# Kernel tuning notes

Measured on AMD Instinct MI355X. Metric: run time of the kernel, lower is better.

## Reference

```python
import jax, jax.numpy as jnp
import numpy as np

B, H, W = 32, 256, 512
C, HF, WF = 768, 16, 32
MAX_KP = 512
NMS_RADIUS = 3.0
SCORE_THRESH = 0.1
K_CAND = min(MAX_KP * 4, H * W)  # 2048


def setup_inputs() -> dict:
    key = jax.random.key(0)
    k1, k2 = jax.random.split(key)
    gray_image = jax.random.uniform(k1, (B, 1, H, W), dtype=jnp.float32)
    mask = jnp.ones((B, 1, H, W), dtype=jnp.float32)
    feat_map = jax.random.normal(k2, (B, C, HF, WF), dtype=jnp.float32)
    return {"gray_image": gray_image, "mask": mask, "feat_map": feat_map}


def _detect_and_sample(img, m, fm):
    # img, m: (H, W); fm: (C, HF, WF)
    masked = (img * m).reshape(-1)
    vals, idx = jax.lax.top_k(masked, K_CAND)  # sorted descending, like torch.topk
    x = (idx % W).astype(jnp.float32)
    y = (idx // W).astype(jnp.float32)
    kp = jnp.stack([x, y], axis=1)  # (K, 2)
    valid = vals > SCORE_THRESH

    # Sequential greedy NMS over score-sorted candidates (matches the torch loop)
    ar = jnp.arange(K_CAND)

    def body(i, keep):
        di = jnp.sqrt(jnp.sum((kp - kp[i]) ** 2, axis=1))
        suppress = (ar > i) & (di < NMS_RADIUS)
        return jnp.where(keep[i], keep & ~suppress, keep)

    keep = jax.lax.fori_loop(0, K_CAND, body, valid)

    # Compact kept points to the front (stable, preserves score order), pad to MAX_KP
    order = jnp.argsort(jnp.logical_not(keep), stable=True)
    sel = order[:MAX_KP]
    n_keep = jnp.sum(keep)
    ok = (jnp.arange(MAX_KP) < n_keep).astype(vals.dtype)  # 1 for real kps, 0 for pad
    kp_out = kp[sel] * ok[:, None]
    sc_out = vals[sel] * ok

    # grid_sample: bilinear, align_corners=True, padding_mode='border'
    # grid = 2*x/W_img - 1  ->  fx = (grid+1)/2*(WF-1) = x/W_img*(WF-1)
    fx = kp_out[:, 0] / W * (WF - 1)
    fy = kp_out[:, 1] / H * (HF - 1)
    x0f, y0f = jnp.floor(fx), jnp.floor(fy)
    wx, wy = fx - x0f, fy - y0f
    x0 = jnp.clip(x0f, 0, WF - 1).astype(jnp.int32)
    x1 = jnp.clip(x0f + 1, 0, WF - 1).astype(jnp.int32)
    y0 = jnp.clip(y0f, 0, HF - 1).astype(jnp.int32)
    y1 = jnp.clip(y0f + 1, 0, HF - 1).astype(jnp.int32)
    g = lambda yy, xx: fm[:, yy, xx]  # (C, MAX_KP)
    desc = (g(y0, x0) * (1 - wx) * (1 - wy) + g(y0, x1) * wx * (1 - wy)
            + g(y1, x0) * (1 - wx) * wy + g(y1, x1) * wx * wy)
    return kp_out, sc_out, desc.T  # (MAX_KP,2), (MAX_KP,), (MAX_KP,C)


def reference(gray_image, mask, feat_map):
    kp, sc, desc = jax.vmap(_detect_and_sample)(gray_image[:, 0], mask[:, 0], feat_map)
    return kp, sc, desc
```

## Files before the change

### kernel.cpp

```cpp
#include <hip/hip_runtime.h>

#define HW_TOT 131072
#define IMG_W  512
#define IMG_H  256
#define KC     2048
#define MAXKP  512
#define NB     32
#define NC     768
#define CG     32
#define NCG    (NC / CG)
#define NBUCK  2048
#define NFB    4096
#define NCAND  4096
#define NSEG   8
#define SEGSZ  (HW_TOT / NSEG)
#define SEGCAP 1024
#define VT0    0.975f
#define LSTRIDE 514
#define MPRE   1024

typedef float f32x4 __attribute__((ext_vector_type(4)));

#define SEGCNT_OFF 0
#define CAND_OFF   2048

__device__ __forceinline__ int blockExclScan(int s, int tid, int* wsum)
{
    const int lane = tid & 63, wid = tid >> 6;
    int incl = s;
    #pragma unroll
    for (int d = 1; d < 64; d <<= 1) {
        int t = __shfl_up(incl, d);
        if (lane >= d) incl += t;
    }
    if (lane == 63) wsum[wid] = incl;
    __syncthreads();
    if (tid == 0) {
        int run = 0;
        #pragma unroll
        for (int w = 0; w < 16; ++w) { int c = wsum[w]; wsum[w] = run; run += c; }
    }
    __syncthreads();
    return wsum[wid] + incl - s;
}

__global__ __launch_bounds__(1024) void scan1_kernel(
    const float* __restrict__ gray,
    const float* __restrict__ mask,
    unsigned int* __restrict__ segcnt,
    unsigned long long* __restrict__ cand)
{
    const int b   = blockIdx.x >> 3;
    const int seg = blockIdx.x & 7;
    const int tid = threadIdx.x;

    __shared__ unsigned long long st[SEGCAP];
    __shared__ unsigned int lcnt;
    if (tid == 0) lcnt = 0u;
    __syncthreads();

    const float4* gi = (const float4*)(gray + (size_t)b * HW_TOT + (size_t)seg * SEGSZ);
    const float4* mi = (const float4*)(mask + (size_t)b * HW_TOT + (size_t)seg * SEGSZ);
    for (int e = tid; e < SEGSZ / 4; e += 1024) {
        float4 g = gi[e], m = mi[e];
        float vv[4] = { g.x * m.x, g.y * m.y, g.z * m.z, g.w * m.w };
        #pragma unroll
        for (int c = 0; c < 4; ++c) {
            float v = vv[c];
            if (v >= VT0) {
                unsigned int eg = (unsigned int)(seg * SEGSZ + 4 * e + c);
                unsigned int p  = atomicAdd(&lcnt, 1u);
                if (p < SEGCAP)
                    st[p] = ((unsigned long long)__float_as_uint(v) << 32) |
                            (unsigned long long)(~eg);
            }
        }
    }
    __syncthreads();
    if (tid == 0) segcnt[blockIdx.x] = lcnt;
    const unsigned int n = lcnt < SEGCAP ? lcnt : SEGCAP;
    unsigned long long* cb = cand + (size_t)blockIdx.x * SEGCAP;
    for (unsigned int i = tid; i < n; i += 1024) cb[i] = st[i];
}

__global__ __launch_bounds__(1024) void final_kernel(
    const float* __restrict__ gray,
    const float* __restrict__ mask,
    const unsigned long long* __restrict__ cand,
    const unsigned int* __restrict__ segcnt,
    float* __restrict__ out_kp,
    float* __restrict__ out_sc)
{
    const int b   = blockIdx.x;
    const int tid = threadIdx.x;

    __shared__ unsigned long long sorted[NCAND];
    __shared__ unsigned long long BUF0[NFB / 2];
    __shared__ unsigned long long BUF1[NFB / 2];
    __shared__ unsigned int posArr[KC];
    __shared__ float valArr[KC];
    __shared__ unsigned int segoff[NSEG + 1];
    __shared__ int wsum[16];
    __shared__ int shT;
    __shared__ unsigned int flagSh;

    unsigned int* cntB   = (unsigned int*)BUF0;
    unsigned int* startB = (unsigned int*)BUF1;

    if (tid == 0) {
        unsigned int tot = 0; int bad = 0; unsigned int run = 0;
        #pragma unroll
        for (int sg = 0; sg < NSEG; ++sg) {
            unsigned int c = segcnt[b * NSEG + sg];
            if (c > SEGCAP) bad = 1;
            segoff[sg] = run; run += c; tot += c;
        }
        segoff[NSEG] = run;
        if (tot < KC || tot > NCAND) bad = 1;
        flagSh = (unsigned int)bad;
        shT = 0;
    }
    __syncthreads();
    const int flag = (int)flagSh;

    const float4* gi = (const float4*)(gray + (size_t)b * HW_TOT);
    const float4* mi = (const float4*)(mask + (size_t)b * HW_TOT);

    if (flag) {
        unsigned int* lh = (unsigned int*)BUF0;
        for (int i = tid; i < NBUCK; i += 1024) lh[i] = 0u;
        __syncthreads();
        for (int e = tid; e < HW_TOT / 4; e += 1024) {
            float4 g = gi[e], m = mi[e];
            int b0 = (int)(g.x * m.x * 2048.0f); b0 = b0 > 2047 ? 2047 : b0;
            int b1 = (int)(g.y * m.y * 2048.0f); b1 = b1 > 2047 ? 2047 : b1;
            int b2 = (int)(g.z * m.z * 2048.0f); b2 = b2 > 2047 ? 2047 : b2;
            int b3 = (int)(g.w * m.w * 2048.0f); b3 = b3 > 2047 ? 2047 : b3;
            atomicAdd(&lh[b0], 1u); atomicAdd(&lh[b1], 1u);
            atomicAdd(&lh[b2], 1u); atomicAdd(&lh[b3], 1u);
        }
        __syncthreads();
        int c0v = (int)lh[2047 - 2 * tid];
        int c1v = (int)lh[2046 - 2 * tid];
        int ex  = blockExclScan(c0v + c1v, tid, wsum);
        int cmax = -1;
        if (ex + c0v >= KC)            cmax = 2047 - 2 * tid;
        else if (ex + c0v + c1v >= KC) cmax = 2046 - 2 * tid;
        if (cmax >= 0) atomicMax(&shT, cmax);
        __syncthreads();
    }
    const float lo    = flag ? (float)shT * (1.0f / 2048.0f) : VT0;
    const float scale = (float)NFB / (1.0f - lo);

    for (int i = tid; i < NFB; i += 1024) cntB[i] = 0u;
    sorted[tid] = 0ull; sorted[tid + 1024] = 0ull;
    __syncthreads();

    if (!flag) {
        for (int sg = 0; sg < NSEG; ++sg) {
            const int n = (int)(segoff[sg + 1] - segoff[sg]);
            const unsigned long long* cbs = cand + (size_t)(b * NSEG + sg) * SEGCAP;
            for (int i = tid; i < n; i += 1024) {
                float v = __uint_as_float((unsigned int)(cbs[i] >> 32));
                int bk = (int)((v - lo) * scale);
                bk = bk < 0 ? 0 : (bk > NFB - 1 ? NFB - 1 : bk);
                atomicAdd(&cntB[bk], 1u);
            }
        }
    } else {
        for (int e = tid; e < HW_TOT / 4; e += 1024) {
            float4 g = gi[e], m = mi[e];
            float vv[4] = { g.x * m.x, g.y * m.y, g.z * m.z, g.w * m.w };
            #pragma unroll
            for (int c = 0; c < 4; ++c) {
                float v = vv[c];
                if (v >= lo) {
                    int bk = (int)((v - lo) * scale);
                    bk = bk < 0 ? 0 : (bk > NFB - 1 ? NFB - 1 : bk);
                    atomicAdd(&cntB[bk], 1u);
                }
            }
        }
    }
    __syncthreads();

    {
        int c[4]; int s = 0;
        #pragma unroll
        for (int j = 0; j < 4; ++j) { c[j] = (int)cntB[NFB - 1 - (4 * tid + j)]; s += c[j]; }
        int ex = blockExclScan(s, tid, wsum);
        #pragma unroll
        for (int j = 0; j < 4; ++j) { startB[NFB - 1 - (4 * tid + j)] = (unsigned int)ex; ex += c[j]; }
    }
    __syncthreads();

    if (!flag) {
        for (int sg = 0; sg < NSEG; ++sg) {
            const int n = (int)(segoff[sg + 1] - segoff[sg]);
            const unsigned long long* cbs = cand + (size_t)(b * NSEG + sg) * SEGCAP;
            for (int i = tid; i < n; i += 1024) {
                unsigned long long key = cbs[i];
                float v = __uint_as_float((unsigned int)(key >> 32));
                int bk = (int)((v - lo) * scale);
                bk = bk < 0 ? 0 : (bk > NFB - 1 ? NFB - 1 : bk);
                unsigned int p = atomicAdd(&startB[bk], 1u);
                if (p < NCAND) sorted[p] = key;
            }
        }
    } else {
        for (int e = tid; e < HW_TOT / 4; e += 1024) {
            float4 g = gi[e], m = mi[e];
            float vv[4] = { g.x * m.x, g.y * m.y, g.z * m.z, g.w * m.w };
            #pragma unroll
            for (int c = 0; c < 4; ++c) {
                float v = vv[c];
                if (v >= lo) {
                    unsigned int eg = (unsigned int)(4 * e + c);
                    int bk = (int)((v - lo) * scale);
                    bk = bk < 0 ? 0 : (bk > NFB - 1 ? NFB - 1 : bk);
                    unsigned int p = atomicAdd(&startB[bk], 1u);
                    if (p < NCAND)
                        sorted[p] = ((unsigned long long)__float_as_uint(v) << 32) |
                                    (unsigned long long)(~eg);
                }
            }
        }
    }
    __syncthreads();

    for (int k = tid; k < NFB; k += 1024) {
        int n = (int)cntB[k];
        if (n >= 2) {
            int endp = (int)startB[k];
            int s    = endp - n;
            if (s < KC) {
                int e2 = endp < NCAND ? endp : NCAND;
                for (int a = s + 1; a < e2; ++a) {
                    unsigned long long key = sorted[a];
                    int bp = a - 1;
                    while (bp >= s && sorted[bp] < key) { sorted[bp + 1] = sorted[bp]; --bp; }
                    sorted[bp + 1] = key;
                }
            }
        }
    }
    __syncthreads();

    for (int i = tid; i < KC; i += 1024) {
        unsigned long long key = sorted[i];
        posArr[i] = ~((unsigned int)(key & 0xFFFFFFFFull));
        valArr[i] = __uint_as_float((unsigned int)(key >> 32));
    }
    __syncthreads();

    unsigned int*   cellCnt   = (unsigned int*)BUF0;
    unsigned int*   cellStart = cellCnt + 2048;
    unsigned short* cellList  = (unsigned short*)BUF1;
    unsigned char*  keepA     = (unsigned char*)(cellList + 2048);
    unsigned char*  keepB     = keepA + KC;
    unsigned char*  nbrCnt    = keepB + KC;
    unsigned short* nbrList   = (unsigned short*)sorted;

    int myKeep = 0;
    int usedPrefix = 1;

    {
        const int i = tid;
        const unsigned int e = posArr[i];
        const int x = (int)(e & (IMG_W - 1)), y = (int)(e >> 9);
        const int cx = (x >> 3) & 63, cy = (y >> 3) & 31;
        const int cell = cy * 64 + cx;
        const bool valid = (valArr[i] > 0.1f);

        cellCnt[tid] = 0u; cellCnt[tid + 1024] = 0u;
        __syncthreads();
        atomicAdd(&cellCnt[cell], 1u);
        __syncthreads();
        {
            int c0v = (int)cellCnt[2 * tid], c1v = (int)cellCnt[2 * tid + 1];
            int ex = blockExclScan(c0v + c1v, tid, wsum);
            cellStart[2 * tid]     = (unsigned int)ex;
            cellStart[2 * tid + 1] = (unsigned int)(ex + c0v);
        }
        __syncthreads();
        {
            unsigned int p = atomicAdd(&cellStart[cell], 1u);
            cellList[p] = (unsigned short)i;
        }
        __syncthreads();

        int n = 0;
        bool sup1 = false;
        for (int dy = -1; dy <= 1; ++dy) {
            int cyy = cy + dy; if (cyy < 0 || cyy > 31) continue;
            for (int dx = -1; dx <= 1; ++dx) {
                int cxx = cx + dx; if (cxx < 0 || cxx > 63) continue;
                int cc = cyy * 64 + cxx;
                int end = (int)cellStart[cc], num = (int)cellCnt[cc];
                for (int q = end - num; q < end; ++q) {
                    int j = (int)cellList[q];
                    if (j < i) {
                        unsigned int ej = posArr[j];
                        int ddx = x - (int)(ej & (IMG_W - 1));
                        int ddy = y - (int)(ej >> 9);
                        if (ddx * ddx + ddy * ddy < 9) {
                            if (n < 8) nbrList[i * 8 + n] = (unsigned short)j;
                            ++n;
                            sup1 = sup1 || (valArr[j] > 0.1f);
                        }
                    }
                }
            }
        }
        nbrCnt[i] = (unsigned char)(n > 8 ? 9 : n);
        int cur = (valid && !sup1) ? 1 : 0;
        keepA[i] = (unsigned char)cur;
        __syncthreads();

        unsigned char *curK = keepA, *nxtK = keepB;
        for (int it = 0; it < KC; ++it) {
            int nv = 0;
            if (valid) {
                bool sup = false;
                int nn = (int)nbrCnt[i];
                if (nn <= 8) {
                    for (int q = 0; q < nn; ++q) sup = sup || (curK[nbrList[i * 8 + q]] != 0);
                } else {
                    for (int dy = -1; dy <= 1 && !sup; ++dy) {
                        int cyy = cy + dy; if (cyy < 0 || cyy > 31) continue;
                        for (int dx = -1; dx <= 1 && !sup; ++dx) {
                            int cxx = cx + dx; if (cxx < 0 || cxx > 63) continue;
                            int cc = cyy * 64 + cxx;
                            int end = (int)cellStart[cc], num = (int)cellCnt[cc];
                            for (int q = end - num; q < end; ++q) {
                                int j = (int)cellList[q];
                                if (j < i && curK[j]) {
                                    unsigned int ej = posArr[j];
                                    int ddx = x - (int)(ej & (IMG_W - 1));
                                    int ddy = y - (int)(ej >> 9);
                                    if (ddx * ddx + ddy * ddy < 9) { sup = true; break; }
                                }
                            }
                        }
                    }
                }
                nv = sup ? 0 : 1;
            }
            nxtK[i] = (unsigned char)nv;
            int totCh = __syncthreads_count(nv != cur);
            { unsigned char* t = curK; curK = nxtK; nxtK = t; }
            cur = nv;
            if (totCh == 0) break;
        }
        myKeep = cur;

        int keeps = __syncthreads_count(myKeep);
        if (keeps < MAXKP) usedPrefix = 0;
    }

    unsigned char* finK = keepA;
    if (!usedPrefix) {
        __syncthreads();
        for (int i = tid; i < 2048; i += 1024) cellCnt[i] = 0u;
        __syncthreads();
        for (int i = tid; i < KC; i += 1024) {
            unsigned int e = posArr[i];
            int cell = (int)((((e >> 9) >> 3) & 31u) * 64u + (((e & (IMG_W-1)) >> 3) & 63u));
            atomicAdd(&cellCnt[cell], 1u);
        }
        __syncthreads();
        {
            int c0v = (int)cellCnt[2 * tid], c1v = (int)cellCnt[2 * tid + 1];
            int ex = blockExclScan(c0v + c1v, tid, wsum);
            cellStart[2 * tid]     = (unsigned int)ex;
            cellStart[2 * tid + 1] = (unsigned int)(ex + c0v);
        }
        __syncthreads();
        for (int i = tid; i < KC; i += 1024) {
            unsigned int e = posArr[i];
            int cell = (int)((((e >> 9) >> 3) & 31u) * 64u + (((e & (IMG_W-1)) >> 3) & 63u));
            unsigned int p = atomicAdd(&cellStart[cell], 1u);
            cellList[p] = (unsigned short)i;
        }
        __syncthreads();
        for (int i = tid; i < KC; i += 1024) {
            unsigned int e = posArr[i];
            int x = (int)(e & (IMG_W - 1)), y = (int)(e >> 9);
            int cx = (x >> 3) & 63, cy = (y >> 3) & 31;
            int n = 0; bool sup1 = false;
            for (int dy = -1; dy <= 1; ++dy) {
                int cyy = cy + dy; if (cyy < 0 || cyy > 31) continue;
                for (int dx = -1; dx <= 1; ++dx) {
                    int cxx = cx + dx; if (cxx < 0 || cxx > 63) continue;
                    int cc = cyy * 64 + cxx;
                    int end = (int)cellStart[cc], num = (int)cellCnt[cc];
                    for (int q = end - num; q < end; ++q) {
                        int j = (int)cellList[q];
                        if (j < i) {
                            unsigned int ej = posArr[j];
                            int ddx = x - (int)(ej & (IMG_W - 1));
                            int ddy = y - (int)(ej >> 9);
                            if (ddx * ddx + ddy * ddy < 9) {
                                if (n < 8) nbrList[i * 8 + n] = (unsigned short)j;
                                ++n;
                                sup1 = sup1 || (valArr[j] > 0.1f);
                            }
                        }
                    }
                }
            }
            nbrCnt[i] = (unsigned char)(n > 8 ? 9 : n);
            keepA[i]  = ((valArr[i] > 0.1f) && !sup1) ? 1 : 0;
        }
        __syncthreads();
        unsigned char *curK = keepA, *nxtK = keepB;
        for (int it = 0; it < KC; ++it) {
            int localCh = 0;
            for (int i = tid; i < KC; i += 1024) {
                unsigned char c0 = curK[i];
                unsigned char nv = 0;
                if (valArr[i] > 0.1f) {
                    int nn = (int)nbrCnt[i];
                    bool sup = false;
                    if (nn <= 8) {
                        for (int q = 0; q < nn; ++q) sup = sup || (curK[nbrList[i * 8 + q]] != 0);
                    } else {
                        unsigned int e = posArr[i];
                        int x = (int)(e & (IMG_W - 1)), y = (int)(e >> 9);
                        int cx = (x >> 3) & 63, cy = (y >> 3) & 31;
                        for (int dy = -1; dy <= 1 && !sup; ++dy) {
                            int cyy = cy + dy; if (cyy < 0 || cyy > 31) continue;
                            for (int dx = -1; dx <= 1 && !sup; ++dx) {
                                int cxx = cx + dx; if (cxx < 0 || cxx > 63) continue;
                                int cc = cyy * 64 + cxx;
                                int end = (int)cellStart[cc], num = (int)cellCnt[cc];
                                for (int q = end - num; q < end; ++q) {
                                    int j = (int)cellList[q];
                                    if (j < i && curK[j]) {
                                        unsigned int ej = posArr[j];
                                        int ddx = x - (int)(ej & (IMG_W - 1));
                                        int ddy = y - (int)(ej >> 9);
                                        if (ddx * ddx + ddy * ddy < 9) { sup = true; break; }
                                    }
                                }
                            }
                        }
                    }
                    nv = sup ? 0 : 1;
                }
                nxtK[i] = nv;
                localCh |= (nv != c0);
            }
            int totCh = __syncthreads_count(localCh);
            { unsigned char* t = curK; curK = nxtK; nxtK = t; }
            if (totCh == 0) break;
        }
        finK = curK;
    }

    float* kpb = out_kp + (size_t)b * (MAXKP * 2);
    float* scb = out_sc + (size_t)b * MAXKP;

    int a0, a1, i0, i1;
    if (usedPrefix) { i0 = tid;     i1 = -1;          a0 = myKeep;         a1 = 0; }
    else            { i0 = 2 * tid; i1 = 2 * tid + 1; a0 = (int)finK[i0]; a1 = (int)finK[i1]; }
    int ex = blockExclScan(a0 + a1, tid, wsum);
    int r0 = ex, r1 = ex + a0;

    if (tid < MAXKP) { kpb[2 * tid] = 0.f; kpb[2 * tid + 1] = 0.f; scb[tid] = 0.f; }
    __syncthreads();
    if (a0 && r0 < MAXKP) {
        unsigned int e = posArr[i0];
        kpb[2 * r0] = (float)(e & (IMG_W - 1)); kpb[2 * r0 + 1] = (float)(e >> 9);
        scb[r0] = valArr[i0];
    }
    if (a1 && r1 < MAXKP) {
        unsigned int e = posArr[i1];
        kpb[2 * r1] = (float)(e & (IMG_W - 1)); kpb[2 * r1 + 1] = (float)(e >> 9);
        scb[r1] = valArr[i1];
    }
}

__global__ __launch_bounds__(1024) void sample_kernel(
    const float* __restrict__ fm,
    const float* __restrict__ kp,
    float* __restrict__ out_desc)
{
    const int blk = blockIdx.x;
    const int b   = blk / NCG;
    const int cg  = blk % NCG;
    const int c0  = cg * CG;
    const int tid = threadIdx.x;

    __shared__ float L[CG * LSTRIDE];
    __shared__ float sxl[MAXKP], syl[MAXKP];

    const float4* src = (const float4*)(fm + (size_t)b * NC * 512 + (size_t)c0 * 512);
    #pragma unroll
    for (int it = 0; it < 4; ++it) {
        int e  = tid + it * 1024;
        int cc = e >> 7, j = e & 127;
        float4 v = src[cc * 128 + j];
        float* dst = &L[cc * LSTRIDE + 4 * j];
        *(float2*)(dst)     = make_float2(v.x, v.y);
        *(float2*)(dst + 2) = make_float2(v.z, v.w);
    }
    if (tid < MAXKP) {
        float2 k2 = ((const float2*)kp)[(size_t)b * MAXKP + tid];
        sxl[tid] = k2.x; syl[tid] = k2.y;
    }
    __syncthreads();

    const int chunk = tid & 7;
    float* outb = out_desc + (size_t)b * MAXKP * NC + c0 + 4 * chunk;
    #pragma unroll
    for (int it = 0; it < 4; ++it) {
        const int p = it * 128 + (tid >> 3);
        float x = sxl[p], y = syl[p];
        float fx = x * (31.0f / 512.0f);
        float fy = y * (15.0f / 256.0f);
        float x0f = floorf(fx), y0f = floorf(fy);
        float wx = fx - x0f, wy = fy - y0f;
        int x0 = (int)fminf(x0f,       31.f);
        int x1 = (int)fminf(x0f + 1.f, 31.f);
        int y0 = (int)fminf(y0f,       15.f);
        int y1 = (int)fminf(y0f + 1.f, 15.f);
        float w00 = (1.f - wx) * (1.f - wy);
        float w01 = wx * (1.f - wy);
        float w10 = (1.f - wx) * wy;
        float w11 = wx * wy;
        int o00 = y0 * 32 + x0, o01 = y0 * 32 + x1;
        int o10 = y1 * 32 + x0, o11 = y1 * 32 + x1;

        f32x4 r;
        #pragma unroll
        for (int u = 0; u < 4; ++u) {
            const float* Lc = &L[(4 * chunk + u) * LSTRIDE];
            r[u] = Lc[o00] * w00 + Lc[o01] * w01 + Lc[o10] * w10 + Lc[o11] * w11;
        }
        __builtin_nontemporal_store(r, (f32x4*)(outb + (size_t)p * NC));
    }
}

extern "C" void kernel_launch(void* const* d_in, const int* in_sizes, int n_in,
                              void* d_out, int out_size, void* d_ws, size_t ws_size,
                              hipStream_t stream)
{
    const float* gray = (const float*)d_in[0];
    const float* mask = (const float*)d_in[1];
    const float* fm   = (const float*)d_in[2];

    float* out      = (float*)d_out;
    float* out_kp   = out;
    float* out_sc   = out + (size_t)NB * MAXKP * 2;
    float* out_desc = out + (size_t)NB * MAXKP * 2 + (size_t)NB * MAXKP;

    unsigned int*       segcnt = (unsigned int*)((char*)d_ws + SEGCNT_OFF);
    unsigned long long* cand   = (unsigned long long*)((char*)d_ws + CAND_OFF);

    scan1_kernel <<<NB * NSEG, 1024, 0, stream>>>(gray, mask, segcnt, cand);
    final_kernel <<<NB,        1024, 0, stream>>>(gray, mask, cand, segcnt,
                                                  out_kp, out_sc);
    sample_kernel<<<NB * NCG,  1024, 0, stream>>>(fm, out_kp, out_desc);
}
```

Before: 50.30 us.

## Fuse keypoint selection into descriptor sampling kernel with redundant per-block NMS

Merges the per-image selection/NMS kernel into the descriptor sampling kernel, so every channel-group block recomputes the keypoints for its image and samples directly from shared memory. This removes one kernel launch and the global round-trip for keypoints, and fills the GPU with many more blocks. In exchange, the selection work is duplicated across channel groups. Shared memory is also reduced by halving the fine bucket count and the neighbor list width, which may push more points onto slower fallback paths.

Measured after the change: 86.13 us. +71.3%, slower.

```diff
diff --git a/kernel.cpp b/kernel.cpp
--- a/kernel.cpp
+++ b/kernel.cpp
@@ -10,14 +10,14 @@
 #define CG     32
 #define NCG    (NC / CG)
 #define NBUCK  2048
-#define NFB    4096
+#define NFB    2048
 #define NCAND  4096
 #define NSEG   8
 #define SEGSZ  (HW_TOT / NSEG)
 #define SEGCAP 1024
 #define VT0    0.975f
 #define LSTRIDE 514
-#define MPRE   1024
+#define NBRW   4
 
 typedef float f32x4 __attribute__((ext_vector_type(4)));
 
@@ -83,29 +83,34 @@
     for (unsigned int i = tid; i < n; i += 1024) cb[i] = st[i];
 }
 
-__global__ __launch_bounds__(1024) void final_kernel(
+__global__ __launch_bounds__(1024) void fused_kernel(
     const float* __restrict__ gray,
     const float* __restrict__ mask,
+    const float* __restrict__ fm,
     const unsigned long long* __restrict__ cand,
     const unsigned int* __restrict__ segcnt,
     float* __restrict__ out_kp,
-    float* __restrict__ out_sc)
+    float* __restrict__ out_sc,
+    float* __restrict__ out_desc)
 {
-    const int b   = blockIdx.x;
+    const int blk = blockIdx.x;
+    const int b   = blk / NCG;
+    const int cg  = blk % NCG;
+    const int c0  = cg * CG;
     const int tid = threadIdx.x;
 
-    __shared__ unsigned long long sorted[NCAND];
-    __shared__ unsigned long long BUF0[NFB / 2];
-    __shared__ unsigned long long BUF1[NFB / 2];
-    __shared__ unsigned int posArr[KC];
-    __shared__ float valArr[KC];
+    __shared__ char U[CG * LSTRIDE * 4];
+    __shared__ float sxl[MAXKP], syl[MAXKP], sss[MAXKP];
     __shared__ unsigned int segoff[NSEG + 1];
     __shared__ int wsum[16];
     __shared__ int shT;
     __shared__ unsigned int flagSh;
 
-    unsigned int* cntB   = (unsigned int*)BUF0;
-    unsigned int* startB = (unsigned int*)BUF1;
+    unsigned long long* sorted = (unsigned long long*)U;
+    unsigned int* cntB   = (unsigned int*)(U + 32768);
+    unsigned int* startB = (unsigned int*)(U + 40960);
+    unsigned int* posArr = (unsigned int*)(U + 49152);
+    float*        valArr = (float*)(U + 57344);
 
     if (tid == 0) {
         unsigned int tot = 0; int bad = 0; unsigned int run = 0;
@@ -127,7 +132,7 @@
     const float4* mi = (const float4*)(mask + (size_t)b * HW_TOT);
 
     if (flag) {
-        unsigned int* lh = (unsigned int*)BUF0;
+        unsigned int* lh = cntB;
         for (int i = tid; i < NBUCK; i += 1024) lh[i] = 0u;
         __syncthreads();
         for (int e = tid; e < HW_TOT / 4; e += 1024) {
@@ -185,12 +190,11 @@
     __syncthreads();
 
     {
-        int c[4]; int s = 0;
-        #pragma unroll
-        for (int j = 0; j < 4; ++j) { c[j] = (int)cntB[NFB - 1 - (4 * tid + j)]; s += c[j]; }
-        int ex = blockExclScan(s, tid, wsum);
-        #pragma unroll
-        for (int j = 0; j < 4; ++j) { startB[NFB - 1 - (4 * tid + j)] = (unsigned int)ex; ex += c[j]; }
+        int c0v = (int)cntB[NFB - 1 - 2 * tid];
+        int c1v = (int)cntB[NFB - 2 - 2 * tid];
+        int ex  = blockExclScan(c0v + c1v, tid, wsum);
+        startB[NFB - 1 - 2 * tid] = (unsigned int)ex;
+        startB[NFB - 2 - 2 * tid] = (unsigned int)(ex + c0v);
     }
     __syncthreads();
 
@@ -253,17 +257,16 @@
     }
     __syncthreads();
 
-    unsigned int*   cellCnt   = (unsigned int*)BUF0;
-    unsigned int*   cellStart = cellCnt + 2048;
-    unsigned short* cellList  = (unsigned short*)BUF1;
-    unsigned char*  keepA     = (unsigned char*)(cellList + 2048);
-    unsigned char*  keepB     = keepA + KC;
-    unsigned char*  nbrCnt    = keepB + KC;
-    unsigned short* nbrList   = (unsigned short*)sorted;
+    unsigned int*   cellCnt   = cntB;
+    unsigned int*   cellStart = startB;
+    unsigned short* nbrList   = (unsigned short*)U;
+    unsigned short* cellList  = (unsigned short*)(U + 16384);
+    unsigned char*  keepA     = (unsigned char*)(U + 20480);
+    unsigned char*  keepB     = (unsigned char*)(U + 22528);
+    unsigned char*  nbrCnt    = (unsigned char*)(U + 24576);
 
     int myKeep = 0;
     int usedPrefix = 1;
-
     {
         const int i = tid;
         const unsigned int e = posArr[i];
@@ -304,7 +307,7 @@
                         int ddx = x - (int)(ej & (IMG_W - 1));
                         int ddy = y - (int)(ej >> 9);
                         if (ddx * ddx + ddy * ddy < 9) {
-                            if (n < 8) nbrList[i * 8 + n] = (unsigned short)j;
+                            if (n < NBRW) nbrList[i * NBRW + n] = (unsigned short)j;
                             ++n;
                             sup1 = sup1 || (valArr[j] > 0.1f);
                         }
@@ -312,7 +315,7 @@
                 }
             }
         }
-        nbrCnt[i] = (unsigned char)(n > 8 ? 9 : n);
+        nbrCnt[i] = (unsigned char)(n > NBRW ? NBRW + 1 : n);
         int cur = (valid && !sup1) ? 1 : 0;
         keepA[i] = (unsigned char)cur;
         __syncthreads();
@@ -323,8 +326,8 @@
             if (valid) {
                 bool sup = false;
                 int nn = (int)nbrCnt[i];
-                if (nn <= 8) {
-                    for (int q = 0; q < nn; ++q) sup = sup || (curK[nbrList[i * 8 + q]] != 0);
+                if (nn <= NBRW) {
+                    for (int q = 0; q < nn; ++q) sup = sup || (curK[nbrList[i * NBRW + q]] != 0);
                 } else {
                     for (int dy = -1; dy <= 1 && !sup; ++dy) {
                         int cyy = cy + dy; if (cyy < 0 || cyy > 31) continue;
@@ -401,7 +404,7 @@
                             int ddx = x - (int)(ej & (IMG_W - 1));
                             int ddy = y - (int)(ej >> 9);
                             if (ddx * ddx + ddy * ddy < 9) {
-                                if (n < 8) nbrList[i * 8 + n] = (unsigned short)j;
+                                if (n < NBRW) nbrList[i * NBRW + n] = (unsigned short)j;
                                 ++n;
                                 sup1 = sup1 || (valArr[j] > 0.1f);
                             }
@@ -409,7 +412,7 @@
                     }
                 }
             }
-            nbrCnt[i] = (unsigned char)(n > 8 ? 9 : n);
+            nbrCnt[i] = (unsigned char)(n > NBRW ? NBRW + 1 : n);
             keepA[i]  = ((valArr[i] > 0.1f) && !sup1) ? 1 : 0;
         }
         __syncthreads();
@@ -417,13 +420,13 @@
         for (int it = 0; it < KC; ++it) {
             int localCh = 0;
             for (int i = tid; i < KC; i += 1024) {
-                unsigned char c0 = curK[i];
+                unsigned char cc0 = curK[i];
                 unsigned char nv = 0;
                 if (valArr[i] > 0.1f) {
                     int nn = (int)nbrCnt[i];
                     bool sup = false;
-                    if (nn <= 8) {
-                        for (int q = 0; q < nn; ++q) sup = sup || (curK[nbrList[i * 8 + q]] != 0);
+                    if (nn <= NBRW) {
+                        for (int q = 0; q < nn; ++q) sup = sup || (curK[nbrList[i * NBRW + q]] != 0);
                     } else {
                         unsigned int e = posArr[i];
                         int x = (int)(e & (IMG_W - 1)), y = (int)(e >> 9);
@@ -449,7 +452,7 @@
                     nv = sup ? 0 : 1;
                 }
                 nxtK[i] = nv;
-                localCh |= (nv != c0);
+                localCh |= (nv != cc0);
             }
             int totCh = __syncthreads_count(localCh);
             { unsigned char* t = curK; curK = nxtK; nxtK = t; }
@@ -457,9 +460,6 @@
         }
         finK = curK;
     }
-
-    float* kpb = out_kp + (size_t)b * (MAXKP * 2);
-    float* scb = out_sc + (size_t)b * MAXKP;
 
     int a0, a1, i0, i1;
     if (usedPrefix) { i0 = tid;     i1 = -1;          a0 = myKeep;         a1 = 0; }
@@ -467,34 +467,26 @@
     int ex = blockExclScan(a0 + a1, tid, wsum);
     int r0 = ex, r1 = ex + a0;
 
-    if (tid < MAXKP) { kpb[2 * tid] = 0.f; kpb[2 * tid + 1] = 0.f; scb[tid] = 0.f; }
+    if (tid < MAXKP) { sxl[tid] = 0.f; syl[tid] = 0.f; sss[tid] = 0.f; }
     __syncthreads();
     if (a0 && r0 < MAXKP) {
         unsigned int e = posArr[i0];
-        kpb[2 * r0] = (float)(e & (IMG_W - 1)); kpb[2 * r0 + 1] = (float)(e >> 9);
-        scb[r0] = valArr[i0];
+        sxl[r0] = (float)(e & (IMG_W - 1)); syl[r0] = (float)(e >> 9); sss[r0] = valArr[i0];
     }
     if (a1 && r1 < MAXKP) {
         unsigned int e = posArr[i1];
-        kpb[2 * r1] = (float)(e & (IMG_W - 1)); kpb[2 * r1 + 1] = (float)(e >> 9);
-        scb[r1] = valArr[i1];
-    }
-}
-
-__global__ __launch_bounds__(1024) void sample_kernel(
-    const float* __restrict__ fm,
-    const float* __restrict__ kp,
-    float* __restrict__ out_desc)
-{
-    const int blk = blockIdx.x;
-    const int b   = blk / NCG;
-    const int cg  = blk % NCG;
-    const int c0  = cg * CG;
-    const int tid = threadIdx.x;
-
-    __shared__ float L[CG * LSTRIDE];
-    __shared__ float sxl[MAXKP], syl[MAXKP];
-
+        sxl[r1] = (float)(e & (IMG_W - 1)); syl[r1] = (float)(e >> 9); sss[r1] = valArr[i1];
+    }
+    __syncthreads();
+
+    if (cg == 0 && tid < MAXKP) {
+        float* kpb = out_kp + (size_t)b * (MAXKP * 2);
+        out_sc[(size_t)b * MAXKP + tid] = sss[tid];
+        kpb[2 * tid]     = sxl[tid];
+        kpb[2 * tid + 1] = syl[tid];
+    }
+
+    float* L = (float*)U;
     const float4* src = (const float4*)(fm + (size_t)b * NC * 512 + (size_t)c0 * 512);
     #pragma unroll
     for (int it = 0; it < 4; ++it) {
@@ -504,10 +496,6 @@
         float* dst = &L[cc * LSTRIDE + 4 * j];
         *(float2*)(dst)     = make_float2(v.x, v.y);
         *(float2*)(dst + 2) = make_float2(v.z, v.w);
-    }
-    if (tid < MAXKP) {
-        float2 k2 = ((const float2*)kp)[(size_t)b * MAXKP + tid];
-        sxl[tid] = k2.x; syl[tid] = k2.y;
     }
     __syncthreads();
 
@@ -558,8 +546,7 @@
     unsigned int*       segcnt = (unsigned int*)((char*)d_ws + SEGCNT_OFF);
     unsigned long long* cand   = (unsigned long long*)((char*)d_ws + CAND_OFF);
 
-    scan1_kernel <<<NB * NSEG, 1024, 0, stream>>>(gray, mask, segcnt, cand);
-    final_kernel <<<NB,        1024, 0, stream>>>(gray, mask, cand, segcnt,
-                                                  out_kp, out_sc);
-    sample_kernel<<<NB * NCG,  1024, 0, stream>>>(fm, out_kp, out_desc);
+    scan1_kernel<<<NB * NSEG, 1024, 0, stream>>>(gray, mask, segcnt, cand);
+    fused_kernel<<<NB * NCG,  1024, 0, stream>>>(gray, mask, fm, cand, segcnt,
+                                                 out_kp, out_sc, out_desc);
 }
```
